# Kernel optimization log

Measured on AMD Instinct MI355X. Metric: run time of the kernel, lower is better.

## Reference

```python
import jax, jax.numpy as jnp
import numpy as np

Bsz, T, D = 2, 2048, 1024
H_ATTN, HD, WIN = 16, 64, 128
H_SSM, DI, N, DCONV, DTR = 8, 2048, 16, 4, 64
P = DI // H_SSM
DT_MIN, DT_MAX = 1e-4, 1.0
EPS = 1e-6


def setup_inputs() -> dict:
    key = jax.random.key(0)
    ks = jax.random.split(key, 16)
    def g(i, shp, s=0.02):
        return jax.random.normal(ks[i], shp, jnp.float32) * s
    TOT = 2 * DI + DTR + 2 * H_SSM * N
    # dt_bias = inverse_softplus(dt) with dt log-uniform in [dt_min, dt_max]
    dt0 = jnp.exp(jax.random.uniform(ks[14], (H_SSM,), jnp.float32) * (np.log(DT_MAX) - np.log(DT_MIN)) + np.log(DT_MIN))
    dt_bias = dt0 + jnp.log(-jnp.expm1(-dt0))
    return dict(
        x=jax.random.normal(ks[0], (Bsz, T, D), jnp.float32),
        norm1_w=jnp.ones((D,), jnp.float32),
        norm2_w=jnp.ones((D,), jnp.float32),
        Win=g(1, (TOT, D)),
        Wdt=g(2, (H_SSM, DTR)),
        conv_w=g(3, (DI, DCONV), 0.2),
        conv_b=jnp.zeros((DI,), jnp.float32),
        A_log=jnp.log(jnp.broadcast_to(jnp.arange(1, N + 1, dtype=jnp.float32), (H_SSM, N))),
        Dskip=jnp.ones((H_SSM, P), jnp.float32),
        dt_bias=dt_bias,
        ssd_norm_w=jnp.ones((DI,), jnp.float32),
        Wout_ssd=g(4, (D, DI)),
        Wres=g(5, (DI, D)),
        Wq=g(6, (D, D)), Wk=g(7, (D, D)), Wv=g(8, (D, D)), Wo=g(9, (D, D)),
    )


def _rms(x, w):
    return x * jax.lax.rsqrt(jnp.mean(x * x, -1, keepdims=True) + EPS) * w


def _silu(x):
    return x * jax.nn.sigmoid(x)


def _dwconv(x, w, b):
    # causal depthwise conv1d: x [B,T,C], w [C,K], left-pad K-1
    K = w.shape[1]
    xp = jnp.pad(x, ((0, 0), (K - 1, 0), (0, 0)))
    y = sum(xp[:, k:k + x.shape[1], :] * w[:, k] for k in range(K))
    return y + b


def _rope(q, k):
    # q,k: [B,H,T,HD]
    inv = 1.0 / (10000.0 ** (jnp.arange(0, HD, 2, dtype=jnp.float32) / HD))
    t = jnp.arange(q.shape[2], dtype=jnp.float32)
    f = jnp.concatenate([t[:, None] * inv, t[:, None] * inv], -1)  # [T,HD]
    cos, sin = jnp.cos(f), jnp.sin(f)
    def rot(x):
        h = x.shape[-1] // 2
        return jnp.concatenate([-x[..., h:], x[..., :h]], -1)
    return q * cos + rot(q) * sin, k * cos + rot(k) * sin


def _ssd_branch(u, Win, Wdt, conv_w, conv_b, A_log, Dskip, dt_bias, ssd_norm_w, Wout_ssd, Wres):
    B = u.shape[0]
    proj = u @ Win.T  # [B,T,4416]
    xin = proj[..., :DI]
    z = proj[..., DI:2 * DI]
    dtl = proj[..., 2 * DI:2 * DI + DTR]
    o = 2 * DI + DTR
    Bm = proj[..., o:o + H_SSM * N].reshape(B, T, H_SSM, N)
    Cm = proj[..., o + H_SSM * N:].reshape(B, T, H_SSM, N)
    xc = _silu(_dwconv(xin, conv_w, conv_b))
    dt = jnp.clip(jax.nn.softplus(dtl @ Wdt.T + dt_bias), DT_MIN, DT_MAX)  # [B,T,H]
    A = -jnp.exp(A_log)  # [H,N]
    xh = xc.reshape(B, T, H_SSM, P)
    dA = jnp.exp(dt[..., None] * A)  # [B,T,H,N]
    dtB = dt[..., None] * Bm        # [B,T,H,N]

    def step(h, inp):
        dA_t, dtB_t, x_t, C_t = inp
        h = h * dA_t[:, :, None, :] + x_t[..., None] * dtB_t[:, :, None, :]
        y = jnp.einsum('bhpn,bhn->bhp', h, C_t)
        return h, y

    h0 = jnp.zeros((B, H_SSM, P, N), u.dtype)
    _, ys = jax.lax.scan(step, h0, (
        dA.transpose(1, 0, 2, 3), dtB.transpose(1, 0, 2, 3),
        xh.transpose(1, 0, 2, 3), Cm.transpose(1, 0, 2, 3)))
    y = ys.transpose(1, 0, 2, 3) + Dskip * xh  # [B,T,H,P]
    y = y.reshape(B, T, DI) + u @ Wres.T       # residual_proj(d_model->d_inner)
    y = _rms(y * _silu(z), ssd_norm_w)         # fused gated RMSNorm
    return y @ Wout_ssd.T


def _attn(u, Wq, Wk, Wv, Wo):
    B = u.shape[0]
    q = (u @ Wq.T).reshape(B, T, H_ATTN, HD).transpose(0, 2, 1, 3)
    k = (u @ Wk.T).reshape(B, T, H_ATTN, HD).transpose(0, 2, 1, 3)
    v = (u @ Wv.T).reshape(B, T, H_ATTN, HD).transpose(0, 2, 1, 3)
    q, k = _rope(q, k)
    s = jnp.einsum('bhtd,bhsd->bhts', q, k) / np.sqrt(HD).astype(np.float32)
    rel = jnp.arange(T)[:, None] - jnp.arange(T)[None, :]
    allowed = (rel >= 0) & (rel < WIN)  # causal sliding window
    s = jnp.where(allowed, s, jnp.float32(-1e30))
    p = jax.nn.softmax(s, axis=-1)
    y = jnp.einsum('bhts,bhsd->bhtd', p, v)
    return y.transpose(0, 2, 1, 3).reshape(B, T, D) @ Wo.T


def reference(x, norm1_w, norm2_w, Win, Wdt, conv_w, conv_b, A_log, Dskip, dt_bias,
              ssd_norm_w, Wout_ssd, Wres, Wq, Wk, Wv, Wo):
    h = x + _ssd_branch(_rms(x, norm1_w), Win, Wdt, conv_w, conv_b, A_log, Dskip,
                        dt_bias, ssd_norm_w, Wout_ssd, Wres)
    return h + _attn(_rms(h, norm2_w), Wq, Wk, Wv, Wo)
```

## Files before the change

kernel.cpp:

```cpp
#include <hip/hip_runtime.h>
#include <stdint.h>

typedef unsigned short u16;
typedef unsigned int u32;
typedef __attribute__((ext_vector_type(8))) short short8;
typedef __attribute__((ext_vector_type(4))) unsigned short ushort4v;
typedef __attribute__((ext_vector_type(4))) float f32x4;

#define Bsz 2
#define Tn 2048
#define Dm 1024
#define H_ATTN 16
#define HDx 64
#define WINx 128
#define H_SSM 8
#define DIx 2048
#define Nst 16
#define DTRx 64
#define Px 256
#define TOTx 4416
#define TOT2 6464
#define RESOFF 4416
#define OFFC (2*DIx+DTRx+H_SSM*Nst)
#define BT (Bsz*Tn)
#define NCH 32
#define LCH 64

__device__ __forceinline__ float b2f(u16 u){ u32 x = ((u32)u)<<16; float f; __builtin_memcpy(&f,&x,4); return f; }
__device__ __forceinline__ u16 f2b(float f){ u32 x; __builtin_memcpy(&x,&f,4); u32 r = x + 0x7fffu + ((x>>16)&1u); return (u16)(r>>16); }

__device__ __forceinline__ float block_sum256(float v){
  #pragma unroll
  for (int o=32;o;o>>=1) v += __shfl_xor(v,o,64);
  __shared__ float sb[4];
  int wid = threadIdx.x>>6;
  if ((threadIdx.x&63)==0) sb[wid]=v;
  __syncthreads();
  v = sb[0]+sb[1]+sb[2]+sb[3];
  __syncthreads();
  return v;
}

__device__ __forceinline__ void gload_lds16(const void* g, void* l){
  __builtin_amdgcn_global_load_lds((const __attribute__((address_space(1))) void*)g,
                                   (__attribute__((address_space(3))) void*)l, 16, 0, 0);
}

struct CvtArgs { const float* s[7]; u16* d[7]; int n[7]; };
__global__ __launch_bounds__(256) void k_cvt_all(CvtArgs a, int total4){
  int i = blockIdx.x*256 + threadIdx.x;
  if (i >= total4) return;
  int e = i*4;
  #pragma unroll
  for (int j=0;j<7;j++){
    if (e < a.n[j]){
      float4 v = *(const float4*)(a.s[j]+e);
      u16* d = a.d[j]+e;
      d[0]=f2b(v.x); d[1]=f2b(v.y); d[2]=f2b(v.z); d[3]=f2b(v.w);
      return;
    }
    e -= a.n[j];
  }
}

__global__ __launch_bounds__(256) void k_rms1024(const float* __restrict__ src, const float* __restrict__ w,
                                                 u16* __restrict__ dst){
  int row = blockIdx.x, tid = threadIdx.x;
  const float* s = src + (size_t)row*1024;
  float v[4]; float ss=0.f;
  #pragma unroll
  for (int i=0;i<4;i++){ v[i] = s[tid + i*256]; ss += v[i]*v[i]; }
  ss = block_sum256(ss);
  float sc = rsqrtf(ss*(1.0f/1024.0f) + 1e-6f);
  u16* d = dst + (size_t)row*1024;
  #pragma unroll
  for (int i=0;i<4;i++){ int c = tid+i*256; d[c] = f2b(v[i]*sc*w[c]); }
}

#define BKq 64

__global__ __launch_bounds__(512,1)
void k_gemm256(const u16* __restrict__ A, const u16* __restrict__ W,
               u16* __restrict__ C16, int M, int N, int K, int gxx){
  __shared__ u16 lds[2][4][128*64];
  int tid = threadIdx.x, lane = tid&63, wid = tid>>6;
  int bid = blockIdx.x;
  int xcd = bid&7, r = bid>>3;
  int halfg = gxx>>1;
  int row0 = (xcd>>1)<<2, col0 = (xcd&1)*halfg;
  int bx = col0 + (r>>2), by = row0 + (r&3);
  int bm = by*256, bn = bx*256;
  int wr = wid>>2, wcn = wid&3;
  int fr = lane&15, fq = lane>>4;
  f32x4 acc[2][2][4][2];
  #pragma unroll
  for (int a=0;a<2;a++)
    #pragma unroll
    for (int b=0;b<2;b++)
      #pragma unroll
      for (int c=0;c<4;c++)
        #pragma unroll
        for (int d=0;d<2;d++)
          #pragma unroll
          for (int rr=0;rr<4;rr++) acc[a][b][c][d][rr]=0.f;

  auto stageHalf = [&](int b, int q, int tt){
    int k0 = tt*BKq;
    #pragma unroll
    for (int i=0;i<2;i++){
      int idx = i*512 + tid;
      int row = idx>>3, c8 = idx&7;
      const u16* src; int gr;
      if (q < 2){ gr = bm + q*128 + row;     if (gr > M-1) gr = M-1; src = A; }
      else      { gr = bn + (q-2)*128 + row; if (gr > N-1) gr = N-1; src = W; }
      gload_lds16(src + (size_t)gr*K + k0 + ((c8 ^ (row&7)))*8, &lds[b][q][(size_t)idx*8]);
    }
  };
  auto loadA = [&](const u16* aP, short8 (&af)[2][4]){
    #pragma unroll
    for (int kk=0;kk<2;kk++)
      #pragma unroll
      for (int mi=0;mi<4;mi++){
        int row = wr*64 + mi*16 + fr;
        af[kk][mi] = *(const short8*)(aP + row*64 + ((kk*4+fq) ^ (row&7))*8);
      }
  };
  auto loadB = [&](const u16* bP, short8 (&bf)[2][2]){
    #pragma unroll
    for (int kk=0;kk<2;kk++)
      #pragma unroll
      for (int ni=0;ni<2;ni++){
        int row = wcn*32 + ni*16 + fr;
        bf[kk][ni] = *(const short8*)(bP + row*64 + ((kk*4+fq) ^ (row&7))*8);
      }
  };

  int NT = K/BKq;
  stageHalf(0,0,0); stageHalf(0,2,0); stageHalf(0,3,0); stageHalf(0,1,0);

  short8 af[2][4], bf0[2][2], bf1[2][2];
  for (int t=0;t<NT;t++){
    int cb = t&1, nb = cb^1;
    int tn = (t+1 < NT) ? t+1 : t;
    const u16* A0 = &lds[cb][0][0];
    const u16* A1 = &lds[cb][1][0];
    const u16* B0 = &lds[cb][2][0];
    const u16* B1 = &lds[cb][3][0];
    stageHalf(nb,0,tn);
    asm volatile("s_waitcnt vmcnt(6)" ::: "memory");
    __builtin_amdgcn_sched_barrier(0);
    __builtin_amdgcn_s_barrier();
    loadA(A0, af); loadB(B0, bf0);
    asm volatile("s_waitcnt lgkmcnt(0)" ::: "memory");
    __builtin_amdgcn_sched_barrier(0);
    __builtin_amdgcn_s_setprio(1);
    #pragma unroll
    for (int kk=0;kk<2;kk++)
      #pragma unroll
      for (int mi=0;mi<4;mi++)
        #pragma unroll
        for (int ni=0;ni<2;ni++)
          acc[0][0][mi][ni] = __builtin_amdgcn_mfma_f32_16x16x32_bf16(af[kk][mi], bf0[kk][ni], acc[0][0][mi][ni], 0,0,0);
    __builtin_amdgcn_s_setprio(0);
    __builtin_amdgcn_s_barrier();
    stageHalf(nb,2,tn);
    asm volatile("s_waitcnt vmcnt(6)" ::: "memory");
    __builtin_amdgcn_sched_barrier(0);
    __builtin_amdgcn_s_barrier();
    loadB(B1, bf1);
    asm volatile("s_waitcnt lgkmcnt(0)" ::: "memory");
    __builtin_amdgcn_sched_barrier(0);
    __builtin_amdgcn_s_setprio(1);
    #pragma unroll
    for (int kk=0;kk<2;kk++)
      #pragma unroll
      for (int mi=0;mi<4;mi++)
        #pragma unroll
        for (int ni=0;ni<2;ni++)
          acc[0][1][mi][ni] = __builtin_amdgcn_mfma_f32_16x16x32_bf16(af[kk][mi], bf1[kk][ni], acc[0][1][mi][ni], 0,0,0);
    __builtin_amdgcn_s_setprio(0);
    __builtin_amdgcn_s_barrier();
    stageHalf(nb,3,tn);
    asm volatile("s_waitcnt vmcnt(6)" ::: "memory");
    __builtin_amdgcn_sched_barrier(0);
    __builtin_amdgcn_s_barrier();
    loadA(A1, af);
    asm volatile("s_waitcnt lgkmcnt(0)" ::: "memory");
    __builtin_amdgcn_sched_barrier(0);
    __builtin_amdgcn_s_setprio(1);
    #pragma unroll
    for (int kk=0;kk<2;kk++)
      #pragma unroll
      for (int mi=0;mi<4;mi++)
        #pragma unroll
        for (int ni=0;ni<2;ni++)
          acc[1][1][mi][ni] = __builtin_amdgcn_mfma_f32_16x16x32_bf16(af[kk][mi], bf1[kk][ni], acc[1][1][mi][ni], 0,0,0);
    __builtin_amdgcn_s_setprio(0);
    __builtin_amdgcn_s_barrier();
    stageHalf(nb,1,tn);
    asm volatile("s_waitcnt vmcnt(6)" ::: "memory");
    __builtin_amdgcn_sched_barrier(0);
    __builtin_amdgcn_s_barrier();
    __builtin_amdgcn_s_setprio(1);
    #pragma unroll
    for (int kk=0;kk<2;kk++)
      #pragma unroll
      for (int mi=0;mi<4;mi++)
        #pragma unroll
        for (int ni=0;ni<2;ni++)
          acc[1][0][mi][ni] = __builtin_amdgcn_mfma_f32_16x16x32_bf16(af[kk][mi], bf0[kk][ni], acc[1][0][mi][ni], 0,0,0);
    __builtin_amdgcn_s_setprio(0);
    __builtin_amdgcn_s_barrier();
  }
  #pragma unroll
  for (int mh=0;mh<2;mh++)
    #pragma unroll
    for (int nh=0;nh<2;nh++)
      #pragma unroll
      for (int mi=0;mi<4;mi++)
        #pragma unroll
        for (int ni=0;ni<2;ni++){
          int row0o = bm + mh*128 + wr*64 + mi*16 + fq*4;
          int col  = bn + nh*128 + wcn*32 + ni*16 + fr;
          if (col < N){
            #pragma unroll
            for (int rr=0;rr<4;rr++)
              C16[(size_t)(row0o+rr)*N + col] = f2b(acc[mh][nh][mi][ni][rr]);
          }
        }
}

template<int NWC>
__global__ __launch_bounds__(256, (NWC==2?2:3))
void k_gemm(const u16* __restrict__ A, const u16* __restrict__ W,
            float* __restrict__ C, u16* __restrict__ C16, const float* __restrict__ ADD,
            u16* __restrict__ qro, u16* __restrict__ kro, u16* __restrict__ vro,
            int M, int N, int K, int gx, int mode){
  constexpr int BN    = 64*NWC;
  constexpr int ROWS  = 128 + BN;
  constexpr int NLOADS= ROWS/32;
  constexpr int MFRAG = (NWC==2)?4:2;
  __shared__ u16 lds[2][ROWS*64];
  int tid = threadIdx.x, lane = tid&63, wid = tid>>6;
  int nwg = gridDim.x;
  int cpx = nwg>>3;
  int bid = blockIdx.x;
  int swz = (bid&7)*cpx + (bid>>3);
  int fourgx = gx<<2;
  int super = swz / fourgx;
  int r     = swz % fourgx;
  int bx = r >> 2;
  int by = (super<<2) + (r&3);
  int bm = by*128, bn = bx*BN;
  int wc = (NWC==2) ? (wid&1) : 0;
  int wr = (NWC==2) ? (wid>>1) : wid;
  int fr = lane&15, fq = lane>>4;
  int s7 = fr&7;
  f32x4 acc[MFRAG][4];
  #pragma unroll
  for (int mi=0;mi<MFRAG;mi++)
    #pragma unroll
    for (int ni=0;ni<4;ni++)
      #pragma unroll
      for (int rr=0;rr<4;rr++) acc[mi][ni][rr]=0.f;

  auto stage = [&](int buf, int t){
    int k0 = t*BKq;
    #pragma unroll
    for (int i=0;i<NLOADS;i++){
      int chunk = i*256 + tid;
      int row = chunk>>3, c8 = chunk&7;
      const u16* src;
      if (row < 128){ int ra = bm + row; if (ra > M-1) ra = M-1; src = A + (size_t)ra*K; }
      else          { int rb = bn + row-128; if (rb > N-1) rb = N-1; src = W + (size_t)rb*K; }
      gload_lds16(src + k0 + ((c8 ^ (row&7)))*8, &lds[buf][(size_t)chunk*8]);
    }
  };

  int NT = K/BKq;
  stage(0, 0);
  stage(1, 1);
  for (int t=0;t<NT;t++){
    int cur = t&1;
    if (t+1 < NT){
      if constexpr (NWC==2) asm volatile("s_waitcnt vmcnt(8)" ::: "memory");
      else                  asm volatile("s_waitcnt vmcnt(6)" ::: "memory");
    } else {
      asm volatile("s_waitcnt vmcnt(0)" ::: "memory");
    }
    __builtin_amdgcn_sched_barrier(0);
    __builtin_amdgcn_s_barrier();
    #pragma unroll
    for (int kk=0;kk<2;kk++){
      short8 bf4[4], af4[MFRAG];
      int slotb = ((kk*4 + fq) ^ s7)*8;
      #pragma unroll
      for (int ni=0;ni<4;ni++)
        bf4[ni] = *(const short8*)(&lds[cur][(128 + wc*64 + ni*16 + fr)*64 + slotb]);
      #pragma unroll
      for (int mi=0;mi<MFRAG;mi++)
        af4[mi] = *(const short8*)(&lds[cur][(wr*(MFRAG*16) + mi*16 + fr)*64 + slotb]);
      #pragma unroll
      for (int mi=0;mi<MFRAG;mi++)
        #pragma unroll
        for (int ni=0;ni<4;ni++)
          acc[mi][ni] = __builtin_amdgcn_mfma_f32_16x16x32_bf16(af4[mi], bf4[ni], acc[mi][ni], 0,0,0);
    }
    asm volatile("s_waitcnt lgkmcnt(0)" ::: "memory");
    __builtin_amdgcn_sched_barrier(0);
    __builtin_amdgcn_s_barrier();
    if (t+2 < NT) stage(cur, t+2);
  }
  if (mode == 5){
    int sec = bn >> 10;
    int hh  = (bn >> 6) & 15;
    #pragma unroll
    for (int mi=0;mi<MFRAG;mi++){
      #pragma unroll
      for (int rr=0;rr<4;rr++){
        int row = bm + wr*(MFRAG*16) + mi*16 + fq*4 + rr;
        int tt = row & (Tn-1), bb = row >> 11;
        size_t dstb = (((size_t)bb*H_ATTN + hh)*Tn + tt)*64;
        if (sec == 2){
          #pragma unroll
          for (int ni=0;ni<4;ni++)
            vro[dstb + ni*16 + fr] = f2b(acc[mi][ni][rr]);
        } else {
          u16* dst = (sec==0) ? qro : kro;
          #pragma unroll
          for (int ni=0;ni<2;ni++){
            int dh = ni*16 + fr;
            float ang = (float)tt * exp2f(-(float)dh * (13.287712379549449f/32.0f));
            float cs = cosf(ang), sn = sinf(ang);
            float lo = acc[mi][ni][rr], hi = acc[mi][ni+2][rr];
            dst[dstb + dh]      = f2b(lo*cs - hi*sn);
            dst[dstb + dh + 32] = f2b(hi*cs + lo*sn);
          }
        }
      }
    }
    return;
  }
  #pragma unroll
  for (int mi=0;mi<MFRAG;mi++){
    int row0 = bm + wr*(MFRAG*16) + mi*16 + fq*4;
    #pragma unroll
    for (int ni=0;ni<4;ni++){
      int col = bn + wc*64 + ni*16 + fr;
      if (col < N){
        #pragma unroll
        for (int rr=0;rr<4;rr++){
          size_t idx = (size_t)(row0+rr)*N + col;
          float v = acc[mi][ni][rr];
          if (mode == 0)      C[idx] = v;
          else if (mode == 2) C16[idx] = f2b(v);
          else                C[idx] = ADD[idx] + v;
        }
      }
    }
  }
}

__global__ __launch_bounds__(256) void k_dtprep(const u16* __restrict__ proj, const float* __restrict__ Wdt,
      const float* __restrict__ dt_bias, const float* __restrict__ A_log,
      float* __restrict__ dtA, float* __restrict__ dtB){
  int idx = blockIdx.x*256 + threadIdx.x;
  int h = idx & 7; int bt = idx >> 3;
  const u16* dtl  = proj + (size_t)bt*TOT2 + 2*DIx;
  const float* wrow = Wdt + h*64;
  float v = dt_bias[h];
  #pragma unroll
  for (int i8=0;i8<8;i8++){
    short8 dv = *(const short8*)(dtl + i8*8);
    #pragma unroll
    for (int e=0;e<8;e++) v += b2f((u16)dv[e])*wrow[i8*8+e];
  }
  float sp = (v > 20.0f) ? v : log1pf(expf(v));
  float dt = fminf(fmaxf(sp, 1e-4f), 1.0f);
  const u16* bm = proj + (size_t)bt*TOT2 + 2*DIx + DTRx + h*16;
  short8 b0 = *(const short8*)(bm);
  short8 b1 = *(const short8*)(bm+8);
  #pragma unroll
  for (int n=0;n<16;n++){
    float Av = -expf(A_log[h*16+n]);
    float bv = (n<8) ? b2f((u16)b0[n]) : b2f((u16)b1[n-8]);
    dtA[(size_t)idx*16+n] = dt*Av;
    dtB[(size_t)idx*16+n] = dt*bv;
  }
}

__global__ __launch_bounds__(256) void k_scan1(const float* __restrict__ dtA, const float* __restrict__ dtB,
    const u16* __restrict__ proj, const float* __restrict__ cw, const float* __restrict__ cb,
    float* __restrict__ expS, u16* __restrict__ y, float* __restrict__ LS){
  __shared__ float sA[1024], sS[1024], sB[1024], sC[1024];
  int bx = blockIdx.x;
  int c = bx & 31, h = (bx>>5)&7, b = bx>>8;
  int tid = threadIdx.x;
  size_t t0 = (size_t)b*Tn + c*64;
  int j = tid>>2, n0 = (tid&3)*4;
  {
    size_t ga = (t0 + j)*128 + h*16 + n0;
    float4 va = *(const float4*)(dtA + ga);
    float4 vb = *(const float4*)(dtB + ga);
    ushort4v vc = *(const ushort4v*)(proj + (t0 + j)*TOT2 + OFFC + h*16 + n0);
    *(float4*)(&sA[j*16+n0]) = va;
    *(float4*)(&sB[j*16+n0]) = vb;
    sC[j*16+n0+0] = b2f(vc[0]); sC[j*16+n0+1] = b2f(vc[1]);
    sC[j*16+n0+2] = b2f(vc[2]); sC[j*16+n0+3] = b2f(vc[3]);
  }
  __syncthreads();
  if (tid < 16){
    float cum = 0.f;
    for (int jj=0;jj<64;jj++){ cum += sA[jj*16+tid]; sS[jj*16+tid] = cum; }
  }
  __syncthreads();
  {
    float e[4], s4[4];
    #pragma unroll
    for (int i=0;i<4;i++){ e[i] = expf(sA[j*16+n0+i]); s4[i] = expf(sS[j*16+n0+i]); }
    #pragma unroll
    for (int i=0;i<4;i++){ sA[j*16+n0+i] = e[i]; sS[j*16+n0+i] = s4[i]; }
    float4 ev; ev.x=s4[0]; ev.y=s4[1]; ev.z=s4[2]; ev.w=s4[3];
    *(float4*)(expS + (t0+j)*128 + h*16 + n0) = ev;
  }
  __syncthreads();
  float st[16];
  #pragma unroll
  for (int n=0;n<16;n++) st[n]=0.f;
  int ch = h*Px + tid;
  const u16* pxin = proj + t0*TOT2 + ch;
  const u16* pres = proj + t0*TOT2 + RESOFF + ch;
  float w0=cw[ch*4+0], w1=cw[ch*4+1], w2=cw[ch*4+2], w3=cw[ch*4+3];
  float bcv = cb[ch];
  float x3=0.f, x2=0.f, x1=0.f;
  if (c > 0){
    x3 = b2f(pxin[-(ptrdiff_t)3*TOT2]);
    x2 = b2f(pxin[-(ptrdiff_t)2*TOT2]);
    x1 = b2f(pxin[-(ptrdiff_t)TOT2]);
  }
  u16* yp = y + t0*DIx + ch;
  for (int jj=0;jj<64;jj++){
    float x0 = b2f(pxin[(size_t)jj*TOT2]);
    float cv = bcv + x3*w0 + x2*w1 + x1*w2 + x0*w3;
    float x = cv / (1.0f + expf(-cv));
    x3=x2; x2=x1; x1=x0;
    float acc = b2f(pres[(size_t)jj*TOT2]);
    #pragma unroll
    for (int n=0;n<16;n++){ st[n] = st[n]*sA[jj*16+n] + x*sB[jj*16+n]; acc += st[n]*sC[jj*16+n]; }
    yp[(size_t)jj*DIx] = f2b(acc);
  }
  float* ls = LS + ((((size_t)b*8+h)*NCH + c)*Px + tid)*16;
  #pragma unroll
  for (int n=0;n<16;n++) ls[n] = st[n];
}

__global__ __launch_bounds__(256) void k_scan2(const float* __restrict__ expS, const float* __restrict__ LS,
                                               float* __restrict__ H0){
  int blk = blockIdx.x;
  int slice = blk & 15;
  int bh = blk >> 4; int b = bh>>3, h = bh&7;
  int tid = threadIdx.x;
  int ch = slice*16 + (tid>>4);
  int n  = tid & 15;
  float Hs = 0.f;
  for (int c=0;c<NCH;c++){
    float dl = expS[((size_t)b*Tn + c*64 + 63)*128 + h*16 + n];
    size_t base = ((((size_t)b*8+h)*NCH + c)*Px + ch)*16 + n;
    H0[base] = Hs;
    Hs = Hs*dl + LS[base];
  }
}

__global__ __launch_bounds__(256) void k_scan3(const u16* __restrict__ proj, const float* __restrict__ expS,
    const float* __restrict__ H0, const float* __restrict__ cw, const float* __restrict__ cb,
    const float* __restrict__ Dskip, u16* __restrict__ y){
  __shared__ float ce[1024];
  int bx = blockIdx.x; int c = bx&31, h=(bx>>5)&7, b=bx>>8;
  int tid = threadIdx.x;
  size_t t0 = (size_t)b*Tn + c*64;
  int j = tid>>2, n0=(tid&3)*4;
  {
    ushort4v cv = *(const ushort4v*)(proj + (t0+j)*TOT2 + OFFC + h*16 + n0);
    float4 evv = *(const float4*)(expS + (t0+j)*128 + h*16 + n0);
    ce[j*16+n0+0] = b2f(cv[0])*evv.x; ce[j*16+n0+1] = b2f(cv[1])*evv.y;
    ce[j*16+n0+2] = b2f(cv[2])*evv.z; ce[j*16+n0+3] = b2f(cv[3])*evv.w;
  }
  __syncthreads();
  float h0[16];
  size_t base = ((((size_t)b*8+h)*NCH + c)*Px + tid)*16;
  #pragma unroll
  for (int n=0;n<16;n++) h0[n] = H0[base+n];
  int ch = h*Px + tid;
  float dsk = Dskip[ch];
  const u16* pxin = proj + t0*TOT2 + ch;
  float w0=cw[ch*4+0], w1=cw[ch*4+1], w2=cw[ch*4+2], w3=cw[ch*4+3];
  float bcv = cb[ch];
  float x3=0.f, x2=0.f, x1=0.f;
  if (c > 0){
    x3 = b2f(pxin[-(ptrdiff_t)3*TOT2]);
    x2 = b2f(pxin[-(ptrdiff_t)2*TOT2]);
    x1 = b2f(pxin[-(ptrdiff_t)TOT2]);
  }
  u16* yp = y + t0*DIx + ch;
  for (int jj=0;jj<64;jj++){
    float x0 = b2f(pxin[(size_t)jj*TOT2]);
    float cv = bcv + x3*w0 + x2*w1 + x1*w2 + x0*w3;
    float x = cv / (1.0f + expf(-cv));
    x3=x2; x2=x1; x1=x0;
    float f = 0.f;
    #pragma unroll
    for (int n=0;n<16;n++) f += ce[jj*16+n]*h0[n];
    size_t yi = (size_t)jj*DIx;
    yp[yi] = f2b(b2f(yp[yi]) + f + dsk*x);
  }
}

__global__ __launch_bounds__(256) void k_gatedrms(const u16* __restrict__ y, const u16* __restrict__ proj,
     const float* __restrict__ w, u16* __restrict__ yn){
  int row = blockIdx.x, tid = threadIdx.x;
  const u16* yr = y + (size_t)row*DIx;
  const u16* zr = proj + (size_t)row*TOT2 + DIx;
  float v[8]; float ss=0.f;
  #pragma unroll
  for (int i=0;i<8;i++){
    int cidx = tid + i*256;
    float z = b2f(zr[cidx]);
    float g = b2f(yr[cidx]) * (z / (1.0f + expf(-z)));
    v[i]=g; ss += g*g;
  }
  ss = block_sum256(ss);
  float sc = rsqrtf(ss*(1.0f/2048.0f) + 1e-6f);
  u16* d = yn + (size_t)row*DIx;
  #pragma unroll
  for (int i=0;i<8;i++){ int cidx=tid+i*256; d[cidx] = f2b(v[i]*sc*w[cidx]); }
}

__global__ __launch_bounds__(256) void k_addrms(const float* __restrict__ x, const float* __restrict__ sout,
     const float* __restrict__ w, float* __restrict__ hbuf, u16* __restrict__ u2){
  int row=blockIdx.x, tid=threadIdx.x;
  float v[4]; float ss=0.f;
  #pragma unroll
  for (int i=0;i<4;i++){
    int cidx = tid + i*256;
    size_t idx = (size_t)row*1024 + cidx;
    float hv = x[idx] + sout[idx];
    hbuf[idx]=hv; v[i]=hv; ss+=hv*hv;
  }
  ss = block_sum256(ss);
  float sc = rsqrtf(ss*(1.0f/1024.0f)+1e-6f);
  #pragma unroll
  for (int i=0;i<4;i++){ int cidx=tid+i*256; u2[(size_t)row*1024+cidx] = f2b(v[i]*sc*w[cidx]); }
}

#define QT 64
#define KSPAN 192
__device__ __forceinline__ u32 swz128a(int row, int b){
  return (u32)((row*128 + b) ^ ((((row&7)^((row>>3)&7)))<<4));
}
__device__ __forceinline__ u32 swz384a(int row, int b){
  return (u32)((row*384 + b) ^ ((((row&7)^((row>>3)&7)))<<4));
}

__global__ __launch_bounds__(256) void k_attn_mfma(const u16* __restrict__ qr, const u16* __restrict__ kr,
    const u16* __restrict__ vr, u16* __restrict__ ya){
  __shared__ u16 bufK[KSPAN*64];
  __shared__ u16 bufV[64*KSPAN];
  int tid = threadIdx.x, lane = tid&63, wid = tid>>6;
  int fr = lane&15, fq = lane>>4;
  int blk = blockIdx.x;
  int qt = blk & 31, bh = blk >> 5;
  int t0 = qt*QT;
  size_t rowbase = (size_t)bh*Tn;
  char* cK = (char*)bufK;
  char* cV = (char*)bufV;

  #pragma unroll
  for (int it=0; it<6; ++it){
    int chunk = it*256 + tid;
    int row = chunk>>3, c8 = chunk&7;
    int sg = t0 - 128 + row;
    if (sg >= 0){
      short8 v = *(const short8*)(kr + (rowbase+sg)*64 + c8*8);
      *(short8*)(cK + swz128a(row, c8*16)) = v;
    }
  }
  #pragma unroll
  for (int it=0; it<6; ++it){
    int idx = it*256 + tid;
    int s = idx>>3, c8 = idx&7, d0 = c8*8;
    int sg = t0 - 128 + s;
    short8 v;
    if (sg >= 0) v = *(const short8*)(vr + (rowbase+sg)*64 + d0);
    else         v = short8{0,0,0,0,0,0,0,0};
    #pragma unroll
    for (int e=0;e<8;e++)
      *(u16*)(cV + swz384a(d0+e, s*2)) = (u16)v[e];
  }
  __syncthreads();

  f32x4 acc[12];
  #pragma unroll
  for (int j=0;j<12;j++)
    #pragma unroll
    for (int r=0;r<4;r++) acc[j][r]=0.f;
  #pragma unroll
  for (int kk=0;kk<2;kk++){
    short8 aq = *(const short8*)(qr + (rowbase + t0 + wid*16 + fr)*64 + kk*32 + fq*8);
    #pragma unroll
    for (int j=0;j<12;j++){
      short8 bk = *(const short8*)(cK + swz128a(j*16+fr, kk*64 + fq*16));
      acc[j] = __builtin_amdgcn_mfma_f32_16x16x32_bf16(aq, bk, acc[j], 0,0,0);
    }
  }

  float p[12][4];
  int cb = lane&15;
  #pragma unroll
  for (int r=0;r<4;r++){
    int rq = wid*16 + (lane>>4)*4 + r;
    float m = -3.0e38f;
    #pragma unroll
    for (int j=0;j<12;j++){
      int c = j*16 + cb;
      bool allowed = (c > rq) && (c <= rq+128) && (c >= 128 - t0);
      float v = allowed ? acc[j][r]*0.125f : -3.0e38f;
      p[j][r] = v;
      m = fmaxf(m, v);
    }
    #pragma unroll
    for (int o=1;o<16;o<<=1) m = fmaxf(m, __shfl_xor(m, o, 64));
    float sum = 0.f;
    #pragma unroll
    for (int j=0;j<12;j++){ float e = __expf(p[j][r]-m); p[j][r]=e; sum += e; }
    #pragma unroll
    for (int o=1;o<16;o<<=1) sum += __shfl_xor(sum, o, 64);
    float inv = 1.0f/sum;
    #pragma unroll
    for (int j=0;j<12;j++) p[j][r] *= inv;
  }
  __syncthreads();

  #pragma unroll
  for (int r=0;r<4;r++){
    int rq = wid*16 + (lane>>4)*4 + r;
    #pragma unroll
    for (int j=0;j<12;j++){
      *(u16*)(cK + swz384a(rq, (j*16+cb)*2)) = f2b(p[j][r]);
    }
  }
  __syncthreads();

  f32x4 acc2[4];
  #pragma unroll
  for (int f=0;f<4;f++)
    #pragma unroll
    for (int r=0;r<4;r++) acc2[f][r]=0.f;
  #pragma unroll
  for (int kk=0;kk<6;kk++){
    short8 ap = *(const short8*)(cK + swz384a(wid*16 + fr, kk*64 + fq*16));
    #pragma unroll
    for (int f=0;f<4;f++){
      short8 bv = *(const short8*)(cV + swz384a(f*16+fr, kk*64 + fq*16));
      acc2[f] = __builtin_amdgcn_mfma_f32_16x16x32_bf16(ap, bv, acc2[f], 0,0,0);
    }
  }
  int b = bh >> 4, h = bh & 15;
  #pragma unroll
  for (int f=0;f<4;f++){
    int d = f*16 + cb;
    #pragma unroll
    for (int r=0;r<4;r++){
      int q = t0 + wid*16 + (lane>>4)*4 + r;
      ya[((size_t)b*Tn + q)*Dm + h*64 + d] = f2b(acc2[f][r]);
    }
  }
}

extern "C" void kernel_launch(void* const* d_in, const int* in_sizes, int n_in,
                              void* d_out, int out_size, void* d_ws, size_t ws_size,
                              hipStream_t stream) {
  const float* x        = (const float*)d_in[0];
  const float* norm1_w  = (const float*)d_in[1];
  const float* norm2_w  = (const float*)d_in[2];
  const float* Win      = (const float*)d_in[3];
  const float* Wdt      = (const float*)d_in[4];
  const float* conv_w   = (const float*)d_in[5];
  const float* conv_b   = (const float*)d_in[6];
  const float* A_log    = (const float*)d_in[7];
  const float* Dskip    = (const float*)d_in[8];
  const float* dt_bias  = (const float*)d_in[9];
  const float* ssd_norm = (const float*)d_in[10];
  const float* Wout_ssd = (const float*)d_in[11];
  const float* Wres     = (const float*)d_in[12];
  const float* Wq       = (const float*)d_in[13];
  const float* Wk       = (const float*)d_in[14];
  const float* Wv       = (const float*)d_in[15];
  const float* Wo       = (const float*)d_in[16];

  char* ws = (char*)d_ws;
  size_t off = 0;
  auto alloc = [&](size_t bytes){ size_t r = off; off += (bytes + 255) & ~(size_t)255; return r; };

  size_t o_WinB  = alloc((size_t)TOTx*Dm*2);
  size_t o_WresB = alloc((size_t)DIx*Dm*2);
  size_t o_WoutB = alloc((size_t)Dm*DIx*2);
  size_t o_WqB   = alloc((size_t)Dm*Dm*2);
  size_t o_WkB   = alloc((size_t)Dm*Dm*2);
  size_t o_WvB   = alloc((size_t)Dm*Dm*2);
  size_t o_WoB   = alloc((size_t)Dm*Dm*2);
  size_t o_u1    = alloc((size_t)BT*Dm*2);
  size_t o_proj  = alloc((size_t)BT*TOT2*2);
  size_t o_sout  = alloc((size_t)BT*Dm*4);
  size_t o_dtA   = alloc((size_t)BT*H_SSM*Nst*4);
  size_t o_dtB   = alloc((size_t)BT*H_SSM*Nst*4);
  size_t o_expS  = alloc((size_t)BT*H_SSM*Nst*4);
  size_t o_LS    = alloc((size_t)Bsz*H_SSM*NCH*Px*Nst*4);
  size_t o_H0    = alloc((size_t)Bsz*H_SSM*NCH*Px*Nst*4);
  size_t o_y     = alloc((size_t)BT*DIx*2);
  size_t o_yn    = alloc((size_t)BT*DIx*2);
  size_t o_hb    = alloc((size_t)BT*Dm*4);
  size_t o_qr    = alloc((size_t)Bsz*H_ATTN*Tn*HDx*2);
  size_t o_kr    = alloc((size_t)Bsz*H_ATTN*Tn*HDx*2);

  u16* WinB  = (u16*)(ws + o_WinB);
  u16* WoutB = (u16*)(ws + o_WoutB);
  u16* WqB   = (u16*)(ws + o_WqB);
  u16* u1    = (u16*)(ws + o_u1);
  u16* projb = (u16*)(ws + o_proj);
  float* dtA  = (float*)(ws + o_dtA);
  float* dtB  = (float*)(ws + o_dtB);
  float* expS = (float*)(ws + o_expS);
  float* LS   = (float*)(ws + o_LS);
  float* H0   = (float*)(ws + o_H0);
  u16*   ybuf16 = (u16*)(ws + o_y);
  u16*   yn   = (u16*)(ws + o_yn);
  float* hb   = (float*)(ws + o_hb);
  float* sout = (float*)(ws + o_sout);
  u16* qr = (u16*)(ws + o_qr);
  u16* kr = (u16*)(ws + o_kr);
  u16* vr = u1;
  u16* yatt = (u16*)(ws + o_y);

  {
    CvtArgs a;
    a.s[0]=Win;  a.d[0]=WinB;  a.n[0]=TOTx*Dm;
    a.s[1]=Wres; a.d[1]=(u16*)(ws + o_WresB); a.n[1]=DIx*Dm;
    a.s[2]=Wout_ssd; a.d[2]=WoutB; a.n[2]=Dm*DIx;
    a.s[3]=Wq; a.d[3]=WqB; a.n[3]=Dm*Dm;
    a.s[4]=Wk; a.d[4]=(u16*)(ws + o_WkB); a.n[4]=Dm*Dm;
    a.s[5]=Wv; a.d[5]=(u16*)(ws + o_WvB); a.n[5]=Dm*Dm;
    a.s[6]=Wo; a.d[6]=(u16*)(ws + o_WoB); a.n[6]=Dm*Dm;
    int total4 = (a.n[0]+a.n[1]+a.n[2]+a.n[3]+a.n[4]+a.n[5]+a.n[6])/4;
    k_cvt_all<<<dim3((total4+255)/256), dim3(256), 0, stream>>>(a, total4);
  }

  k_rms1024<<<dim3(BT), dim3(256), 0, stream>>>(x, norm1_w, u1);
  k_gemm256<<<dim3(16*26), dim3(512), 0, stream>>>(u1, WinB, projb, BT, TOT2, Dm, 26);
  k_dtprep<<<dim3(BT*H_SSM/256), dim3(256), 0, stream>>>(projb, Wdt, dt_bias, A_log, dtA, dtB);
  k_scan1<<<dim3(Bsz*H_SSM*NCH), dim3(256), 0, stream>>>(dtA, dtB, projb, conv_w, conv_b, expS, ybuf16, LS);
  k_scan2<<<dim3(Bsz*H_SSM*16), dim3(256), 0, stream>>>(expS, LS, H0);
  k_scan3<<<dim3(Bsz*H_SSM*NCH), dim3(256), 0, stream>>>(projb, expS, H0, conv_w, conv_b, Dskip, ybuf16);
  k_gatedrms<<<dim3(BT), dim3(256), 0, stream>>>(ybuf16, projb, ssd_norm, yn);
  k_gemm<1><<<dim3(16*32), dim3(256), 0, stream>>>(yn, WoutB, sout, nullptr, nullptr,
                                                   nullptr, nullptr, nullptr, BT, Dm, DIx, 16, 0);
  k_addrms<<<dim3(BT), dim3(256), 0, stream>>>(x, sout, norm2_w, hb, (u16*)(ws + o_yn));
  u16* u2p = (u16*)(ws + o_yn);
  k_gemm<1><<<dim3(48*32), dim3(256), 0, stream>>>(u2p, WqB, nullptr, nullptr, nullptr,
                                                   qr, kr, vr, BT, 3*Dm, Dm, 48, 5);
  k_attn_mfma<<<dim3(Bsz*H_ATTN*(Tn/QT)), dim3(256), 0, stream>>>(qr, kr, vr, yatt);
  k_gemm<1><<<dim3(16*32), dim3(256), 0, stream>>>(yatt, (u16*)(ws + o_WoB), (float*)d_out, nullptr, hb,
                                                   nullptr, nullptr, nullptr, BT, Dm, Dm, 16, 3);
  (void)in_sizes; (void)n_in; (void)out_size; (void)ws_size;
}
```

Baseline: 321.0 us.

## Fuse dt prep into scan1, move D-skip to scan1, store intermediates in bf16

```diff
diff --git a/kernel.cpp b/kernel.cpp
--- a/kernel.cpp
+++ b/kernel.cpp
@@ -233,7 +233,7 @@
 template<int NWC>
 __global__ __launch_bounds__(256, (NWC==2?2:3))
 void k_gemm(const u16* __restrict__ A, const u16* __restrict__ W,
-            float* __restrict__ C, u16* __restrict__ C16, const float* __restrict__ ADD,
+            float* __restrict__ C, u16* __restrict__ C16, const u16* __restrict__ ADD16,
             u16* __restrict__ qro, u16* __restrict__ kro, u16* __restrict__ vro,
             int M, int N, int K, int gx, int mode){
   constexpr int BN    = 64*NWC;
@@ -354,59 +354,47 @@
           float v = acc[mi][ni][rr];
           if (mode == 0)      C[idx] = v;
           else if (mode == 2) C16[idx] = f2b(v);
-          else                C[idx] = ADD[idx] + v;
+          else                C[idx] = b2f(ADD16[idx]) + v;
         }
       }
     }
   }
 }
 
-__global__ __launch_bounds__(256) void k_dtprep(const u16* __restrict__ proj, const float* __restrict__ Wdt,
-      const float* __restrict__ dt_bias, const float* __restrict__ A_log,
-      float* __restrict__ dtA, float* __restrict__ dtB){
-  int idx = blockIdx.x*256 + threadIdx.x;
-  int h = idx & 7; int bt = idx >> 3;
-  const u16* dtl  = proj + (size_t)bt*TOT2 + 2*DIx;
-  const float* wrow = Wdt + h*64;
-  float v = dt_bias[h];
-  #pragma unroll
-  for (int i8=0;i8<8;i8++){
-    short8 dv = *(const short8*)(dtl + i8*8);
-    #pragma unroll
-    for (int e=0;e<8;e++) v += b2f((u16)dv[e])*wrow[i8*8+e];
-  }
-  float sp = (v > 20.0f) ? v : log1pf(expf(v));
-  float dt = fminf(fmaxf(sp, 1e-4f), 1.0f);
-  const u16* bm = proj + (size_t)bt*TOT2 + 2*DIx + DTRx + h*16;
-  short8 b0 = *(const short8*)(bm);
-  short8 b1 = *(const short8*)(bm+8);
-  #pragma unroll
-  for (int n=0;n<16;n++){
-    float Av = -expf(A_log[h*16+n]);
-    float bv = (n<8) ? b2f((u16)b0[n]) : b2f((u16)b1[n-8]);
-    dtA[(size_t)idx*16+n] = dt*Av;
-    dtB[(size_t)idx*16+n] = dt*bv;
-  }
-}
-
-__global__ __launch_bounds__(256) void k_scan1(const float* __restrict__ dtA, const float* __restrict__ dtB,
-    const u16* __restrict__ proj, const float* __restrict__ cw, const float* __restrict__ cb,
+__global__ __launch_bounds__(256) void k_scan1(
+    const u16* __restrict__ proj, const float* __restrict__ Wdt,
+    const float* __restrict__ dt_bias, const float* __restrict__ A_log,
+    const float* __restrict__ cw, const float* __restrict__ cb,
+    const float* __restrict__ Dskip,
     float* __restrict__ expS, u16* __restrict__ y, float* __restrict__ LS){
   __shared__ float sA[1024], sS[1024], sB[1024], sC[1024];
   int bx = blockIdx.x;
   int c = bx & 31, h = (bx>>5)&7, b = bx>>8;
   int tid = threadIdx.x;
   size_t t0 = (size_t)b*Tn + c*64;
-  int j = tid>>2, n0 = (tid&3)*4;
+  int j = tid>>2, q = tid&3, n0 = q*4;
   {
-    size_t ga = (t0 + j)*128 + h*16 + n0;
-    float4 va = *(const float4*)(dtA + ga);
-    float4 vb = *(const float4*)(dtB + ga);
-    ushort4v vc = *(const ushort4v*)(proj + (t0 + j)*TOT2 + OFFC + h*16 + n0);
-    *(float4*)(&sA[j*16+n0]) = va;
-    *(float4*)(&sB[j*16+n0]) = vb;
-    sC[j*16+n0+0] = b2f(vc[0]); sC[j*16+n0+1] = b2f(vc[1]);
-    sC[j*16+n0+2] = b2f(vc[2]); sC[j*16+n0+3] = b2f(vc[3]);
+    const u16* dtl = proj + (t0+j)*TOT2 + 2*DIx + q*16;
+    short8 d0 = *(const short8*)(dtl);
+    short8 d1 = *(const short8*)(dtl+8);
+    const float* wrow = Wdt + h*64 + q*16;
+    float part = 0.f;
+    #pragma unroll
+    for (int e=0;e<8;e++){ part += b2f((u16)d0[e])*wrow[e]; part += b2f((u16)d1[e])*wrow[8+e]; }
+    part += __shfl_xor(part, 1, 64);
+    part += __shfl_xor(part, 2, 64);
+    float v = part + dt_bias[h];
+    float sp = (v > 20.0f) ? v : log1pf(expf(v));
+    float dt = fminf(fmaxf(sp, 1e-4f), 1.0f);
+    ushort4v bm4 = *(const ushort4v*)(proj + (t0+j)*TOT2 + 2*DIx + DTRx + h*16 + n0);
+    ushort4v cm4 = *(const ushort4v*)(proj + (t0+j)*TOT2 + OFFC + h*16 + n0);
+    #pragma unroll
+    for (int i=0;i<4;i++){
+      float Av = -expf(A_log[h*16 + n0 + i]);
+      sA[j*16+n0+i] = dt*Av;
+      sB[j*16+n0+i] = dt*b2f(bm4[i]);
+      sC[j*16+n0+i] = b2f(cm4[i]);
+    }
   }
   __syncthreads();
   if (tid < 16){
@@ -432,6 +420,7 @@
   const u16* pres = proj + t0*TOT2 + RESOFF + ch;
   float w0=cw[ch*4+0], w1=cw[ch*4+1], w2=cw[ch*4+2], w3=cw[ch*4+3];
   float bcv = cb[ch];
+  float dsk = Dskip[ch];
   float x3=0.f, x2=0.f, x1=0.f;
   if (c > 0){
     x3 = b2f(pxin[-(ptrdiff_t)3*TOT2]);
@@ -444,7 +433,7 @@
     float cv = bcv + x3*w0 + x2*w1 + x1*w2 + x0*w3;
     float x = cv / (1.0f + expf(-cv));
     x3=x2; x2=x1; x1=x0;
-    float acc = b2f(pres[(size_t)jj*TOT2]);
+    float acc = b2f(pres[(size_t)jj*TOT2]) + dsk*x;
     #pragma unroll
     for (int n=0;n<16;n++){ st[n] = st[n]*sA[jj*16+n] + x*sB[jj*16+n]; acc += st[n]*sC[jj*16+n]; }
     yp[(size_t)jj*DIx] = f2b(acc);
@@ -472,8 +461,7 @@
 }
 
 __global__ __launch_bounds__(256) void k_scan3(const u16* __restrict__ proj, const float* __restrict__ expS,
-    const float* __restrict__ H0, const float* __restrict__ cw, const float* __restrict__ cb,
-    const float* __restrict__ Dskip, u16* __restrict__ y){
+    const float* __restrict__ H0, u16* __restrict__ y){
   __shared__ float ce[1024];
   int bx = blockIdx.x; int c = bx&31, h=(bx>>5)&7, b=bx>>8;
   int tid = threadIdx.x;
@@ -491,27 +479,13 @@
   #pragma unroll
   for (int n=0;n<16;n++) h0[n] = H0[base+n];
   int ch = h*Px + tid;
-  float dsk = Dskip[ch];
-  const u16* pxin = proj + t0*TOT2 + ch;
-  float w0=cw[ch*4+0], w1=cw[ch*4+1], w2=cw[ch*4+2], w3=cw[ch*4+3];
-  float bcv = cb[ch];
-  float x3=0.f, x2=0.f, x1=0.f;
-  if (c > 0){
-    x3 = b2f(pxin[-(ptrdiff_t)3*TOT2]);
-    x2 = b2f(pxin[-(ptrdiff_t)2*TOT2]);
-    x1 = b2f(pxin[-(ptrdiff_t)TOT2]);
-  }
   u16* yp = y + t0*DIx + ch;
   for (int jj=0;jj<64;jj++){
-    float x0 = b2f(pxin[(size_t)jj*TOT2]);
-    float cv = bcv + x3*w0 + x2*w1 + x1*w2 + x0*w3;
-    float x = cv / (1.0f + expf(-cv));
-    x3=x2; x2=x1; x1=x0;
     float f = 0.f;
     #pragma unroll
     for (int n=0;n<16;n++) f += ce[jj*16+n]*h0[n];
     size_t yi = (size_t)jj*DIx;
-    yp[yi] = f2b(b2f(yp[yi]) + f + dsk*x);
+    yp[yi] = f2b(b2f(yp[yi]) + f);
   }
 }
 
@@ -535,16 +509,17 @@
   for (int i=0;i<8;i++){ int cidx=tid+i*256; d[cidx] = f2b(v[i]*sc*w[cidx]); }
 }
 
-__global__ __launch_bounds__(256) void k_addrms(const float* __restrict__ x, const float* __restrict__ sout,
-     const float* __restrict__ w, float* __restrict__ hbuf, u16* __restrict__ u2){
+__global__ __launch_bounds__(256) void k_addrms(const float* __restrict__ x, const u16* __restrict__ sout16,
+     const float* __restrict__ w, u16* __restrict__ hb16, u16* __restrict__ u2){
   int row=blockIdx.x, tid=threadIdx.x;
   float v[4]; float ss=0.f;
   #pragma unroll
   for (int i=0;i<4;i++){
     int cidx = tid + i*256;
     size_t idx = (size_t)row*1024 + cidx;
-    float hv = x[idx] + sout[idx];
-    hbuf[idx]=hv; v[i]=hv; ss+=hv*hv;
+    float hv = x[idx] + b2f(sout16[idx]);
+    hb16[idx] = f2b(hv);
+    v[i]=hv; ss+=hv*hv;
   }
   ss = block_sum256(ss);
   float sc = rsqrtf(ss*(1.0f/1024.0f)+1e-6f);
@@ -710,15 +685,13 @@
   size_t o_WoB   = alloc((size_t)Dm*Dm*2);
   size_t o_u1    = alloc((size_t)BT*Dm*2);
   size_t o_proj  = alloc((size_t)BT*TOT2*2);
-  size_t o_sout  = alloc((size_t)BT*Dm*4);
-  size_t o_dtA   = alloc((size_t)BT*H_SSM*Nst*4);
-  size_t o_dtB   = alloc((size_t)BT*H_SSM*Nst*4);
+  size_t o_sout  = alloc((size_t)BT*Dm*2);
   size_t o_expS  = alloc((size_t)BT*H_SSM*Nst*4);
   size_t o_LS    = alloc((size_t)Bsz*H_SSM*NCH*Px*Nst*4);
   size_t o_H0    = alloc((size_t)Bsz*H_SSM*NCH*Px*Nst*4);
   size_t o_y     = alloc((size_t)BT*DIx*2);
   size_t o_yn    = alloc((size_t)BT*DIx*2);
-  size_t o_hb    = alloc((size_t)BT*Dm*4);
+  size_t o_hb    = alloc((size_t)BT*Dm*2);
   size_t o_qr    = alloc((size_t)Bsz*H_ATTN*Tn*HDx*2);
   size_t o_kr    = alloc((size_t)Bsz*H_ATTN*Tn*HDx*2);
 
@@ -727,15 +700,13 @@
   u16* WqB   = (u16*)(ws + o_WqB);
   u16* u1    = (u16*)(ws + o_u1);
   u16* projb = (u16*)(ws + o_proj);
-  float* dtA  = (float*)(ws + o_dtA);
-  float* dtB  = (float*)(ws + o_dtB);
   float* expS = (float*)(ws + o_expS);
   float* LS   = (float*)(ws + o_LS);
   float* H0   = (float*)(ws + o_H0);
   u16*   ybuf16 = (u16*)(ws + o_y);
   u16*   yn   = (u16*)(ws + o_yn);
-  float* hb   = (float*)(ws + o_hb);
-  float* sout = (float*)(ws + o_sout);
+  u16*   hb16 = (u16*)(ws + o_hb);
+  u16*   sout16 = (u16*)(ws + o_sout);
   u16* qr = (u16*)(ws + o_qr);
   u16* kr = (u16*)(ws + o_kr);
   u16* vr = u1;
@@ -756,19 +727,19 @@
 
   k_rms1024<<<dim3(BT), dim3(256), 0, stream>>>(x, norm1_w, u1);
   k_gemm256<<<dim3(16*26), dim3(512), 0, stream>>>(u1, WinB, projb, BT, TOT2, Dm, 26);
-  k_dtprep<<<dim3(BT*H_SSM/256), dim3(256), 0, stream>>>(projb, Wdt, dt_bias, A_log, dtA, dtB);
-  k_scan1<<<dim3(Bsz*H_SSM*NCH), dim3(256), 0, stream>>>(dtA, dtB, projb, conv_w, conv_b, expS, ybuf16, LS);
+  k_scan1<<<dim3(Bsz*H_SSM*NCH), dim3(256), 0, stream>>>(projb, Wdt, dt_bias, A_log,
+                                                         conv_w, conv_b, Dskip, expS, ybuf16, LS);
   k_scan2<<<dim3(Bsz*H_SSM*16), dim3(256), 0, stream>>>(expS, LS, H0);
-  k_scan3<<<dim3(Bsz*H_SSM*NCH), dim3(256), 0, stream>>>(projb, expS, H0, conv_w, conv_b, Dskip, ybuf16);
+  k_scan3<<<dim3(Bsz*H_SSM*NCH), dim3(256), 0, stream>>>(projb, expS, H0, ybuf16);
   k_gatedrms<<<dim3(BT), dim3(256), 0, stream>>>(ybuf16, projb, ssd_norm, yn);
-  k_gemm<1><<<dim3(16*32), dim3(256), 0, stream>>>(yn, WoutB, sout, nullptr, nullptr,
-                                                   nullptr, nullptr, nullptr, BT, Dm, DIx, 16, 0);
-  k_addrms<<<dim3(BT), dim3(256), 0, stream>>>(x, sout, norm2_w, hb, (u16*)(ws + o_yn));
+  k_gemm<1><<<dim3(16*32), dim3(256), 0, stream>>>(yn, WoutB, nullptr, sout16, nullptr,
+                                                   nullptr, nullptr, nullptr, BT, Dm, DIx, 16, 2);
+  k_addrms<<<dim3(BT), dim3(256), 0, stream>>>(x, sout16, norm2_w, hb16, (u16*)(ws + o_yn));
   u16* u2p = (u16*)(ws + o_yn);
   k_gemm<1><<<dim3(48*32), dim3(256), 0, stream>>>(u2p, WqB, nullptr, nullptr, nullptr,
                                                    qr, kr, vr, BT, 3*Dm, Dm, 48, 5);
   k_attn_mfma<<<dim3(Bsz*H_ATTN*(Tn/QT)), dim3(256), 0, stream>>>(qr, kr, vr, yatt);
-  k_gemm<1><<<dim3(16*32), dim3(256), 0, stream>>>(yatt, (u16*)(ws + o_WoB), (float*)d_out, nullptr, hb,
+  k_gemm<1><<<dim3(16*32), dim3(256), 0, stream>>>(yatt, (u16*)(ws + o_WoB), (float*)d_out, nullptr, hb16,
                                                    nullptr, nullptr, nullptr, BT, Dm, Dm, 16, 3);
   (void)in_sizes; (void)n_in; (void)out_size; (void)ws_size;
 }
```

Result: faster. 271.6 us, median of 2 (-15.4%).
